# Performance work log

Measured on AMD Instinct MI355X. Metric: run time of the kernel, lower is better.

The kernel has to match this reference:

```python
import jax, jax.numpy as jnp
import numpy as np

B, T, C, H = 4, 2048, 768, 12
D = C // H  # head dim = 64

def setup_inputs() -> dict:
    key = jax.random.key(0)
    k1, k2, k3 = jax.random.split(key, 3)
    x = jax.random.normal(k1, (B, T, C), dtype=jnp.float32)
    W_attn = jax.random.normal(k2, (C, 3 * C), dtype=jnp.float32) * 0.02
    b_attn = jnp.zeros((3 * C,), dtype=jnp.float32)
    W_proj = jax.random.normal(k3, (C, C), dtype=jnp.float32) * 0.02
    b_proj = jnp.zeros((C,), dtype=jnp.float32)
    return {"x": x, "W_attn": W_attn, "b_attn": b_attn, "W_proj": W_proj, "b_proj": b_proj}

def reference(x, W_attn, b_attn, W_proj, b_proj):
    Bx, Tx, Cx = x.shape
    qkv = x @ W_attn + b_attn                      # [B,T,3C]
    q, k, v = jnp.split(qkv, 3, axis=2)
    q = q.reshape(Bx, Tx, H, D).swapaxes(1, 2)     # [B,H,T,D]
    k = k.reshape(Bx, Tx, H, D).swapaxes(1, 2)
    v = v.reshape(Bx, Tx, H, D).swapaxes(1, 2)
    att = jnp.einsum('bhqd,bhkd->bhqk', q, k) / jnp.sqrt(jnp.float32(D))
    mask = jnp.tril(jnp.ones((Tx, Tx), dtype=bool))
    att = jnp.where(mask, att, -jnp.inf)
    att = jax.nn.softmax(att, axis=-1)
    y = jnp.einsum('bhqk,bhkd->bhqd', att, v)      # [B,H,T,D]
    y = y.swapaxes(1, 2).reshape(Bx, Tx, Cx)
    return y @ W_proj + b_proj
```

## Files before the change

### kernel.cpp

```cpp
#include <hip/hip_runtime.h>
#include <hip/hip_bf16.h>

#define BATCH 4
#define TSEQ  2048
#define CDIM  768
#define HNUM  12
#define DHEAD 64
#define NQKV  (3*CDIM)
#define BTOT  (BATCH*TSEQ)
#define BH    (BATCH*HNUM)

typedef unsigned short u16;
typedef __attribute__((ext_vector_type(8))) __bf16 bf16x8;
typedef __attribute__((ext_vector_type(4))) float f32x4;

#define MFMA16(a,b,c) __builtin_amdgcn_mfma_f32_16x16x32_bf16((a),(b),(c),0,0,0)

__device__ __forceinline__ u16 f2b(float f) {
    union { float f; unsigned u; } v; v.f = f;
    unsigned u = v.u;
    unsigned r = (u + 0x7fffu + ((u >> 16) & 1u)) >> 16;
    return (u16)r;
}

__device__ __forceinline__ unsigned cvtpk(float lo, float hi) {
    unsigned r;
    asm("v_cvt_pk_bf16_f32 %0, %1, %2" : "=v"(r) : "v"(lo), "v"(hi));
    return r;
}

__device__ __forceinline__ float fexp2(float x) {
    float r;
    asm("v_exp_f32 %0, %1" : "=v"(r) : "v"(x));
    return r;
}

__device__ __forceinline__ void gload_lds(const void* g, void* l) {
    __builtin_amdgcn_global_load_lds(
        (const __attribute__((address_space(1))) void*)g,
        (__attribute__((address_space(3))) void*)l, 16, 0, 0);
}

__global__ __launch_bounds__(256) void cast_f32_bf16(
        const float* __restrict__ in, u16* __restrict__ out, int n4) {
    int i = blockIdx.x * blockDim.x + threadIdx.x;
    if (i >= n4) return;
    float4 a = reinterpret_cast<const float4*>(in)[i];
    ushort4 o;
    o.x = f2b(a.x); o.y = f2b(a.y); o.z = f2b(a.z); o.w = f2b(a.w);
    reinterpret_cast<ushort4*>(out)[i] = o;
}

__global__ __launch_bounds__(256) void tcast2(
        const float* __restrict__ Wa, const float* __restrict__ Wp,
        u16* __restrict__ WaT, u16* __restrict__ WpT) {
    __shared__ float tile[32][33];
    const float* in; u16* out; int Cc; int bx = blockIdx.x;
    if (bx < NQKV / 32) { in = Wa; out = WaT; Cc = NQKV; }
    else                { in = Wp; out = WpT; Cc = CDIM; bx -= NQKV / 32; }
    int c0 = bx * 32, r0 = blockIdx.y * 32;
    int tx = threadIdx.x, ty = threadIdx.y;
    #pragma unroll
    for (int i = 0; i < 32; i += 8)
        tile[ty + i][tx] = in[(size_t)(r0 + ty + i) * Cc + c0 + tx];
    __syncthreads();
    #pragma unroll
    for (int i = 0; i < 32; i += 8)
        out[(size_t)(c0 + ty + i) * CDIM + r0 + tx] = f2b(tile[tx][ty + i]);
}

template<int MODE, int NX>
__global__ __launch_bounds__(256) void gemm_bt(
        const u16* __restrict__ A, const u16* __restrict__ Bt,
        const float* __restrict__ bias,
        u16* __restrict__ qb, u16* __restrict__ kb, u16* __restrict__ vtb,
        float* __restrict__ outf, int K) {
    __shared__ u16 sA[2][128 * 32];
    __shared__ u16 sB[2][128 * 32];
    const int tid = threadIdx.x;
    const int lane = tid & 63;
    const int w = tid >> 6;
    const int wr = w >> 1, wc = w & 1;
    const int g = lane >> 4, lq = lane & 15;
    const int cpx = gridDim.x >> 3;
    const int wg = ((int)blockIdx.x & 7) * cpx + ((int)blockIdx.x >> 3);
    const int bx = wg % NX, by = wg / NX;
    const int m0 = by * 128, n0 = bx * 128;

    f32x4 acc[4][4] = {};

    auto stage = [&](int buf, int kt) {
        #pragma unroll
        for (int i = 0; i < 2; ++i) {
            int c = i * 256 + tid;
            int r = c >> 2, s = c & 3;
            int l = s ^ ((r >> 1) & 3);
            gload_lds(A  + (size_t)(m0 + r) * K + kt * 32 + l * 8, &sA[buf][c * 8]);
            gload_lds(Bt + (size_t)(n0 + r) * K + kt * 32 + l * 8, &sB[buf][c * 8]);
        }
    };

    const int KT = K / 32;
    stage(0, 0);
    __syncthreads();
    for (int kt = 0; kt < KT; ++kt) {
        if (kt + 1 < KT) stage((kt + 1) & 1, kt + 1);
        const u16* cA = sA[kt & 1];
        const u16* cB = sB[kt & 1];
        bf16x8 af[4], bfr[4];
        #pragma unroll
        for (int m = 0; m < 4; ++m) {
            int r = wr * 64 + m * 16 + lq;
            af[m] = *(const bf16x8*)&cA[r * 32 + ((g ^ ((r >> 1) & 3)) << 3)];
        }
        #pragma unroll
        for (int n = 0; n < 4; ++n) {
            int r = wc * 64 + n * 16 + lq;
            bfr[n] = *(const bf16x8*)&cB[r * 32 + ((g ^ ((r >> 1) & 3)) << 3)];
        }
        __builtin_amdgcn_s_setprio(1);
        #pragma unroll
        for (int m = 0; m < 4; ++m)
            #pragma unroll
            for (int n = 0; n < 4; ++n)
                acc[m][n] = MFMA16(bfr[n], af[m], acc[m][n]);
        __builtin_amdgcn_s_setprio(0);
        __syncthreads();
    }

    if (MODE == 0) {
        const int which = n0 / CDIM;
        #pragma unroll
        for (int m = 0; m < 4; ++m) {
            const int rg = m0 + wr * 64 + m * 16 + lq;
            const int b = rg >> 11, t = rg & (TSEQ - 1);
            #pragma unroll
            for (int n = 0; n < 4; ++n) {
                const int cg = n0 + wc * 64 + n * 16 + (g << 2);
                const int c  = cg - which * CDIM;
                const int h  = c >> 6, d = c & 63;
                const size_t bh = (size_t)(b * HNUM + h);
                const float4 bv = *(const float4*)&bias[cg];
                const float v0 = acc[m][n][0] + bv.x;
                const float v1 = acc[m][n][1] + bv.y;
                const float v2 = acc[m][n][2] + bv.z;
                const float v3 = acc[m][n][3] + bv.w;
                if (which == 0) {
                    const float s = 0.1803368801111243f;
                    ushort4 pv;
                    pv.x = f2b(v0 * s); pv.y = f2b(v1 * s);
                    pv.z = f2b(v2 * s); pv.w = f2b(v3 * s);
                    *(ushort4*)&qb[(bh * TSEQ + t) * DHEAD + d] = pv;
                } else if (which == 1) {
                    ushort4 pv;
                    pv.x = f2b(v0); pv.y = f2b(v1); pv.z = f2b(v2); pv.w = f2b(v3);
                    *(ushort4*)&kb[(bh * TSEQ + t) * DHEAD + d] = pv;
                } else {
                    vtb[(bh * DHEAD + d + 0) * TSEQ + t] = f2b(v0);
                    vtb[(bh * DHEAD + d + 1) * TSEQ + t] = f2b(v1);
                    vtb[(bh * DHEAD + d + 2) * TSEQ + t] = f2b(v2);
                    vtb[(bh * DHEAD + d + 3) * TSEQ + t] = f2b(v3);
                }
            }
        }
    } else {
        #pragma unroll
        for (int m = 0; m < 4; ++m) {
            const int rg = m0 + wr * 64 + m * 16 + lq;
            #pragma unroll
            for (int n = 0; n < 4; ++n) {
                const int cg = n0 + wc * 64 + n * 16 + (g << 2);
                const float4 bv = *(const float4*)&bias[cg];
                float4 ov;
                ov.x = acc[m][n][0] + bv.x;
                ov.y = acc[m][n][1] + bv.y;
                ov.z = acc[m][n][2] + bv.z;
                ov.w = acc[m][n][3] + bv.w;
                *(float4*)&outf[(size_t)rg * CDIM + cg] = ov;
            }
        }
    }
}

__global__ __launch_bounds__(256, 4) void attn_fwd(
        const u16* __restrict__ qb, const u16* __restrict__ kb,
        const u16* __restrict__ vtb, u16* __restrict__ yb) {
    __shared__ u16 sK[2][64 * 64];
    __shared__ u16 sVt[2][64 * 64];
    const int qt = 31 - (int)(blockIdx.x / BH);
    const int bh = blockIdx.x % BH;
    const int b = bh / HNUM, h = bh % HNUM;
    const int tid = threadIdx.x, lane = tid & 63, w = tid >> 6;
    const int g = lane >> 4, lq = lane & 15;
    const int qlo = qt * 64 + w * 16;
    const u16* qbase = qb  + (size_t)bh * TSEQ * DHEAD;
    const u16* kbase = kb  + (size_t)bh * TSEQ * DHEAD;
    const u16* vbase = vtb + (size_t)bh * DHEAD * TSEQ;

    bf16x8 qf[2];
    #pragma unroll
    for (int ks = 0; ks < 2; ++ks)
        qf[ks] = *(const bf16x8*)&qbase[(size_t)(qlo + lq) * DHEAD + ks * 32 + g * 8];

    union { unsigned u[4]; bf16x8 v; } ones;
    #pragma unroll
    for (int i = 0; i < 4; ++i) ones.u[i] = 0x3f803f80u;

    f32x4 o[4] = {};
    f32x4 ls = {};
    float mx = -__builtin_inff();

    auto STAGE = [&](int buf, int kt) {
        const int k0 = kt << 6;
        #pragma unroll
        for (int i = 0; i < 2; ++i) {
            int chunk = i * 256 + tid;
            int srow = chunk >> 3;
            int cb = ((chunk & 7) << 4) ^ ((srow & 7) << 4);
            gload_lds(kbase + (size_t)(k0 + srow) * DHEAD + (cb >> 1), &sK[buf][chunk * 8]);
            gload_lds(vbase + (size_t)srow * TSEQ + k0 + (cb >> 1),    &sVt[buf][chunk * 8]);
        }
    };

    const int nk = qt + 1;
    STAGE(0, 0);
    __syncthreads();
    for (int kt = 0; kt < nk; ++kt) {
        const int k0 = kt << 6;
        if (kt + 1 < nk) STAGE((kt + 1) & 1, kt + 1);
        const u16* cK = sK[kt & 1];
        const u16* cV = sVt[kt & 1];
        f32x4 s[4];
        #pragma unroll
        for (int n = 0; n < 4; ++n) s[n] = f32x4{0.f, 0.f, 0.f, 0.f};
        __builtin_amdgcn_s_setprio(1);
        #pragma unroll
        for (int n = 0; n < 4; ++n) {
            #pragma unroll
            for (int ks = 0; ks < 2; ++ks) {
                int r = n * 16 + lq;
                int lb = (r * 128 + (ks * 32 + g * 8) * 2) ^ ((r & 7) << 4);
                bf16x8 kf = *(const bf16x8*)((const char*)cK + lb);
                s[n] = MFMA16(kf, qf[ks], s[n]);
            }
        }
        __builtin_amdgcn_s_setprio(0);
        if (k0 + 63 > qlo) {
            const int qa = qlo + lq;
            #pragma unroll
            for (int n = 0; n < 4; ++n)
                #pragma unroll
                for (int j = 0; j < 4; ++j)
                    if (k0 + n * 16 + g * 4 + j > qa) s[n][j] = -__builtin_inff();
        }
        float t0 = fmaxf(fmaxf(s[0][0], s[0][1]), fmaxf(s[0][2], s[0][3]));
        float t1 = fmaxf(fmaxf(s[1][0], s[1][1]), fmaxf(s[1][2], s[1][3]));
        float t2 = fmaxf(fmaxf(s[2][0], s[2][1]), fmaxf(s[2][2], s[2][3]));
        float t3 = fmaxf(fmaxf(s[3][0], s[3][1]), fmaxf(s[3][2], s[3][3]));
        float tmax = fmaxf(fmaxf(t0, t1), fmaxf(t2, t3));
        tmax = fmaxf(tmax, __shfl_xor(tmax, 16));
        tmax = fmaxf(tmax, __shfl_xor(tmax, 32));
        if (__any(tmax > mx + 8.0f)) {
            float mnew = fmaxf(mx, tmax);
            float sc = fexp2(mx - mnew);
            mx = mnew;
            #pragma unroll
            for (int j = 0; j < 4; ++j) {
                float scj = __shfl(sc, (lane & 48) | ((g << 2) + j));
                ls[j] *= scj;
                #pragma unroll
                for (int n = 0; n < 4; ++n) o[n][j] *= scj;
            }
        }
        #pragma unroll
        for (int n = 0; n < 4; ++n)
            #pragma unroll
            for (int j = 0; j < 4; ++j)
                s[n][j] = fexp2(s[n][j] - mx);
        unsigned apk[4], bpk[4];
        #pragma unroll
        for (int n = 0; n < 4; ++n) {
            apk[n] = cvtpk(s[n][0], s[n][1]);
            bpk[n] = cvtpk(s[n][2], s[n][3]);
        }
        const int s0l = lq + ((lane & 16) << 1);
        const bool hi = (lane & 32) != 0;
        #pragma unroll
        for (int ks = 0; ks < 2; ++ks) {
            unsigned A0  = (unsigned)__shfl((int)apk[2 * ks],     s0l);
            unsigned B0  = (unsigned)__shfl((int)bpk[2 * ks],     s0l);
            unsigned A1  = (unsigned)__shfl((int)apk[2 * ks + 1], s0l);
            unsigned B1  = (unsigned)__shfl((int)bpk[2 * ks + 1], s0l);
            unsigned A0h = (unsigned)__shfl((int)apk[2 * ks],     s0l + 16);
            unsigned B0h = (unsigned)__shfl((int)bpk[2 * ks],     s0l + 16);
            unsigned A1h = (unsigned)__shfl((int)apk[2 * ks + 1], s0l + 16);
            unsigned B1h = (unsigned)__shfl((int)bpk[2 * ks + 1], s0l + 16);
            union { unsigned u[4]; bf16x8 v; } pa;
            pa.u[0] = hi ? A1  : A0;
            pa.u[1] = hi ? B1  : B0;
            pa.u[2] = hi ? A1h : A0h;
            pa.u[3] = hi ? B1h : B0h;
            __builtin_amdgcn_s_setprio(1);
            #pragma unroll
            for (int n = 0; n < 4; ++n) {
                int d = n * 16 + lq;
                int lb = (d * 128 + (ks * 32 + g * 8) * 2) ^ ((d & 7) << 4);
                bf16x8 vf = *(const bf16x8*)((const char*)cV + lb);
                o[n] = MFMA16(pa.v, vf, o[n]);
            }
            ls = MFMA16(pa.v, ones.v, ls);
            __builtin_amdgcn_s_setprio(0);
        }
        __syncthreads();
    }

    #pragma unroll
    for (int j = 0; j < 4; ++j) {
        float inv = 1.f / ls[j];
        const int t = qlo + g * 4 + j;
        #pragma unroll
        for (int n = 0; n < 4; ++n) {
            const int c = h * DHEAD + n * 16 + lq;
            yb[((size_t)b * TSEQ + t) * CDIM + c] = f2b(o[n][j] * inv);
        }
    }
}

extern "C" void kernel_launch(void* const* d_in, const int* in_sizes, int n_in,
                              void* d_out, int out_size, void* d_ws, size_t ws_size,
                              hipStream_t stream) {
    const float* x      = (const float*)d_in[0];
    const float* W_attn = (const float*)d_in[1];
    const float* b_attn = (const float*)d_in[2];
    const float* W_proj = (const float*)d_in[3];
    const float* b_proj = (const float*)d_in[4];
    float* out = (float*)d_out;

    u16* ws = (u16*)d_ws;
    u16* xb     = ws;
    u16* yb     = xb;
    u16* WattnT = xb     + (size_t)BTOT * CDIM;
    u16* WprojT = WattnT + (size_t)NQKV * CDIM;
    u16* qb     = WprojT + (size_t)CDIM * CDIM;
    u16* kb     = qb     + (size_t)BH * TSEQ * DHEAD;
    u16* vtb    = kb     + (size_t)BH * TSEQ * DHEAD;

    int n4 = BTOT * CDIM / 4;
    cast_f32_bf16<<<(n4 + 255) / 256, 256, 0, stream>>>(x, xb, n4);
    tcast2<<<dim3(NQKV / 32 + CDIM / 32, CDIM / 32), dim3(32, 8), 0, stream>>>(
        W_attn, W_proj, WattnT, WprojT);

    gemm_bt<0, NQKV / 128><<<dim3((NQKV / 128) * (BTOT / 128)), 256, 0, stream>>>(
        xb, WattnT, b_attn, qb, kb, vtb, nullptr, CDIM);

    attn_fwd<<<dim3((TSEQ / 64) * BH), 256, 0, stream>>>(qb, kb, vtb, yb);

    gemm_bt<1, CDIM / 128><<<dim3((CDIM / 128) * (BTOT / 128)), 256, 0, stream>>>(
        yb, WprojT, b_proj, nullptr, nullptr, nullptr, out, CDIM);
}
```

Before: 141.7 us.

## Double attention query tile per block and merge prep casts into one kernel

The attention kernel now gives each block 128 query rows instead of 64, and each wave handles two 16-row query subtiles. Every K/V tile staged in LDS is therefore reused for twice as many queries, halving K/V global traffic per query, and waves whose rows lie entirely before a key tile skip its compute. The x cast and the weight transpose-casts are merged into one launch to remove a kernel launch. In exchange the grid has half as many blocks, the causal work is less evenly balanced, and register pressure rises, which may reduce occupancy.

```diff
diff --git a/kernel.cpp b/kernel.cpp
--- a/kernel.cpp
+++ b/kernel.cpp
@@ -41,25 +41,31 @@
         (__attribute__((address_space(3))) void*)l, 16, 0, 0);
 }
 
-__global__ __launch_bounds__(256) void cast_f32_bf16(
-        const float* __restrict__ in, u16* __restrict__ out, int n4) {
-    int i = blockIdx.x * blockDim.x + threadIdx.x;
-    if (i >= n4) return;
-    float4 a = reinterpret_cast<const float4*>(in)[i];
-    ushort4 o;
-    o.x = f2b(a.x); o.y = f2b(a.y); o.z = f2b(a.z); o.w = f2b(a.w);
-    reinterpret_cast<ushort4*>(out)[i] = o;
-}
-
-__global__ __launch_bounds__(256) void tcast2(
+#define CAST_BLKS (BTOT * CDIM / 4 / 256)
+#define TA_BLKS   ((NQKV / 32) * (CDIM / 32))
+#define TP_BLKS   ((CDIM / 32) * (CDIM / 32))
+__global__ __launch_bounds__(256) void prep(
+        const float* __restrict__ x, u16* __restrict__ xb,
         const float* __restrict__ Wa, const float* __restrict__ Wp,
         u16* __restrict__ WaT, u16* __restrict__ WpT) {
     __shared__ float tile[32][33];
-    const float* in; u16* out; int Cc; int bx = blockIdx.x;
-    if (bx < NQKV / 32) { in = Wa; out = WaT; Cc = NQKV; }
-    else                { in = Wp; out = WpT; Cc = CDIM; bx -= NQKV / 32; }
-    int c0 = bx * 32, r0 = blockIdx.y * 32;
-    int tx = threadIdx.x, ty = threadIdx.y;
+    const int bx = blockIdx.x, tid = threadIdx.x;
+    if (bx < CAST_BLKS) {
+        int i = bx * 256 + tid;
+        float4 a = reinterpret_cast<const float4*>(x)[i];
+        ushort4 o;
+        o.x = f2b(a.x); o.y = f2b(a.y); o.z = f2b(a.z); o.w = f2b(a.w);
+        reinterpret_cast<ushort4*>(xb)[i] = o;
+        return;
+    }
+    int bz = bx - CAST_BLKS;
+    const float* in; u16* out; int Cc;
+    int nxa = NQKV / 32;
+    int cx, ry;
+    if (bz < TA_BLKS) { in = Wa; out = WaT; Cc = NQKV; cx = bz % nxa; ry = bz / nxa; }
+    else { bz -= TA_BLKS; in = Wp; out = WpT; Cc = CDIM; cx = bz % (CDIM/32); ry = bz / (CDIM/32); }
+    int c0 = cx * 32, r0 = ry * 32;
+    int tx = tid & 31, ty = tid >> 5;
     #pragma unroll
     for (int i = 0; i < 32; i += 8)
         tile[ty + i][tx] = in[(size_t)(r0 + ty + i) * Cc + c0 + tx];
@@ -187,28 +193,31 @@
         const u16* __restrict__ vtb, u16* __restrict__ yb) {
     __shared__ u16 sK[2][64 * 64];
     __shared__ u16 sVt[2][64 * 64];
-    const int qt = 31 - (int)(blockIdx.x / BH);
+    const int qt = 15 - (int)(blockIdx.x / BH);
     const int bh = blockIdx.x % BH;
     const int b = bh / HNUM, h = bh % HNUM;
     const int tid = threadIdx.x, lane = tid & 63, w = tid >> 6;
     const int g = lane >> 4, lq = lane & 15;
-    const int qlo = qt * 64 + w * 16;
+    const int qlo = qt * 128 + w * 32;
     const u16* qbase = qb  + (size_t)bh * TSEQ * DHEAD;
     const u16* kbase = kb  + (size_t)bh * TSEQ * DHEAD;
     const u16* vbase = vtb + (size_t)bh * DHEAD * TSEQ;
 
-    bf16x8 qf[2];
-    #pragma unroll
-    for (int ks = 0; ks < 2; ++ks)
-        qf[ks] = *(const bf16x8*)&qbase[(size_t)(qlo + lq) * DHEAD + ks * 32 + g * 8];
+    bf16x8 qf[2][2];
+    #pragma unroll
+    for (int m = 0; m < 2; ++m)
+        #pragma unroll
+        for (int ks = 0; ks < 2; ++ks)
+            qf[m][ks] = *(const bf16x8*)&qbase[(size_t)(qlo + m * 16 + lq) * DHEAD
+                                               + ks * 32 + g * 8];
 
     union { unsigned u[4]; bf16x8 v; } ones;
     #pragma unroll
     for (int i = 0; i < 4; ++i) ones.u[i] = 0x3f803f80u;
 
-    f32x4 o[4] = {};
-    f32x4 ls = {};
-    float mx = -__builtin_inff();
+    f32x4 o[2][4] = {};
+    f32x4 ls[2] = {};
+    float mx[2] = { -__builtin_inff(), -__builtin_inff() };
 
     auto STAGE = [&](int buf, int kt) {
         const int k0 = kt << 6;
@@ -222,108 +231,132 @@
         }
     };
 
-    const int nk = qt + 1;
+    const int nk = 2 * qt + 2;
     STAGE(0, 0);
     __syncthreads();
     for (int kt = 0; kt < nk; ++kt) {
         const int k0 = kt << 6;
         if (kt + 1 < nk) STAGE((kt + 1) & 1, kt + 1);
-        const u16* cK = sK[kt & 1];
-        const u16* cV = sVt[kt & 1];
-        f32x4 s[4];
-        #pragma unroll
-        for (int n = 0; n < 4; ++n) s[n] = f32x4{0.f, 0.f, 0.f, 0.f};
-        __builtin_amdgcn_s_setprio(1);
-        #pragma unroll
-        for (int n = 0; n < 4; ++n) {
+        if (k0 <= qlo + 31) {
+            const u16* cK = sK[kt & 1];
+            const u16* cV = sVt[kt & 1];
+            f32x4 s[2][4];
+            #pragma unroll
+            for (int m = 0; m < 2; ++m)
+                #pragma unroll
+                for (int n = 0; n < 4; ++n) s[m][n] = f32x4{0.f, 0.f, 0.f, 0.f};
+            __builtin_amdgcn_s_setprio(1);
+            #pragma unroll
+            for (int n = 0; n < 4; ++n) {
+                #pragma unroll
+                for (int ks = 0; ks < 2; ++ks) {
+                    int r = n * 16 + lq;
+                    int lb = (r * 128 + (ks * 32 + g * 8) * 2) ^ ((r & 7) << 4);
+                    bf16x8 kf = *(const bf16x8*)((const char*)cK + lb);
+                    s[0][n] = MFMA16(kf, qf[0][ks], s[0][n]);
+                    s[1][n] = MFMA16(kf, qf[1][ks], s[1][n]);
+                }
+            }
+            __builtin_amdgcn_s_setprio(0);
+            if (k0 + 63 > qlo) {
+                #pragma unroll
+                for (int m = 0; m < 2; ++m) {
+                    const int qa = qlo + m * 16 + lq;
+                    #pragma unroll
+                    for (int n = 0; n < 4; ++n)
+                        #pragma unroll
+                        for (int j = 0; j < 4; ++j)
+                            if (k0 + n * 16 + g * 4 + j > qa) s[m][n][j] = -__builtin_inff();
+                }
+            }
+            float tmax[2];
+            #pragma unroll
+            for (int m = 0; m < 2; ++m) {
+                float t0 = fmaxf(fmaxf(s[m][0][0], s[m][0][1]), fmaxf(s[m][0][2], s[m][0][3]));
+                float t1 = fmaxf(fmaxf(s[m][1][0], s[m][1][1]), fmaxf(s[m][1][2], s[m][1][3]));
+                float t2 = fmaxf(fmaxf(s[m][2][0], s[m][2][1]), fmaxf(s[m][2][2], s[m][2][3]));
+                float t3 = fmaxf(fmaxf(s[m][3][0], s[m][3][1]), fmaxf(s[m][3][2], s[m][3][3]));
+                float tm = fmaxf(fmaxf(t0, t1), fmaxf(t2, t3));
+                tm = fmaxf(tm, __shfl_xor(tm, 16));
+                tm = fmaxf(tm, __shfl_xor(tm, 32));
+                tmax[m] = tm;
+            }
+            if (__any(tmax[0] > mx[0] + 8.0f || tmax[1] > mx[1] + 8.0f)) {
+                #pragma unroll
+                for (int m = 0; m < 2; ++m) {
+                    float mnew = fmaxf(mx[m], tmax[m]);
+                    float sc = fexp2(mx[m] - mnew);
+                    mx[m] = mnew;
+                    #pragma unroll
+                    for (int j = 0; j < 4; ++j) {
+                        float scj = __shfl(sc, (lane & 48) | ((g << 2) + j));
+                        ls[m][j] *= scj;
+                        #pragma unroll
+                        for (int n = 0; n < 4; ++n) o[m][n][j] *= scj;
+                    }
+                }
+            }
+            unsigned apk[2][4], bpk[2][4];
+            #pragma unroll
+            for (int m = 0; m < 2; ++m)
+                #pragma unroll
+                for (int n = 0; n < 4; ++n) {
+                    float p0 = fexp2(s[m][n][0] - mx[m]);
+                    float p1 = fexp2(s[m][n][1] - mx[m]);
+                    float p2 = fexp2(s[m][n][2] - mx[m]);
+                    float p3 = fexp2(s[m][n][3] - mx[m]);
+                    apk[m][n] = cvtpk(p0, p1);
+                    bpk[m][n] = cvtpk(p2, p3);
+                }
+            const int s0l = lq + ((lane & 16) << 1);
+            const bool hi = (lane & 32) != 0;
             #pragma unroll
             for (int ks = 0; ks < 2; ++ks) {
-                int r = n * 16 + lq;
-                int lb = (r * 128 + (ks * 32 + g * 8) * 2) ^ ((r & 7) << 4);
-                bf16x8 kf = *(const bf16x8*)((const char*)cK + lb);
-                s[n] = MFMA16(kf, qf[ks], s[n]);
-            }
-        }
-        __builtin_amdgcn_s_setprio(0);
-        if (k0 + 63 > qlo) {
-            const int qa = qlo + lq;
-            #pragma unroll
-            for (int n = 0; n < 4; ++n)
-                #pragma unroll
-                for (int j = 0; j < 4; ++j)
-                    if (k0 + n * 16 + g * 4 + j > qa) s[n][j] = -__builtin_inff();
-        }
-        float t0 = fmaxf(fmaxf(s[0][0], s[0][1]), fmaxf(s[0][2], s[0][3]));
-        float t1 = fmaxf(fmaxf(s[1][0], s[1][1]), fmaxf(s[1][2], s[1][3]));
-        float t2 = fmaxf(fmaxf(s[2][0], s[2][1]), fmaxf(s[2][2], s[2][3]));
-        float t3 = fmaxf(fmaxf(s[3][0], s[3][1]), fmaxf(s[3][2], s[3][3]));
-        float tmax = fmaxf(fmaxf(t0, t1), fmaxf(t2, t3));
-        tmax = fmaxf(tmax, __shfl_xor(tmax, 16));
-        tmax = fmaxf(tmax, __shfl_xor(tmax, 32));
-        if (__any(tmax > mx + 8.0f)) {
-            float mnew = fmaxf(mx, tmax);
-            float sc = fexp2(mx - mnew);
-            mx = mnew;
-            #pragma unroll
-            for (int j = 0; j < 4; ++j) {
-                float scj = __shfl(sc, (lane & 48) | ((g << 2) + j));
-                ls[j] *= scj;
-                #pragma unroll
-                for (int n = 0; n < 4; ++n) o[n][j] *= scj;
-            }
-        }
-        #pragma unroll
-        for (int n = 0; n < 4; ++n)
-            #pragma unroll
-            for (int j = 0; j < 4; ++j)
-                s[n][j] = fexp2(s[n][j] - mx);
-        unsigned apk[4], bpk[4];
-        #pragma unroll
-        for (int n = 0; n < 4; ++n) {
-            apk[n] = cvtpk(s[n][0], s[n][1]);
-            bpk[n] = cvtpk(s[n][2], s[n][3]);
-        }
-        const int s0l = lq + ((lane & 16) << 1);
-        const bool hi = (lane & 32) != 0;
-        #pragma unroll
-        for (int ks = 0; ks < 2; ++ks) {
-            unsigned A0  = (unsigned)__shfl((int)apk[2 * ks],     s0l);
-            unsigned B0  = (unsigned)__shfl((int)bpk[2 * ks],     s0l);
-            unsigned A1  = (unsigned)__shfl((int)apk[2 * ks + 1], s0l);
-            unsigned B1  = (unsigned)__shfl((int)bpk[2 * ks + 1], s0l);
-            unsigned A0h = (unsigned)__shfl((int)apk[2 * ks],     s0l + 16);
-            unsigned B0h = (unsigned)__shfl((int)bpk[2 * ks],     s0l + 16);
-            unsigned A1h = (unsigned)__shfl((int)apk[2 * ks + 1], s0l + 16);
-            unsigned B1h = (unsigned)__shfl((int)bpk[2 * ks + 1], s0l + 16);
-            union { unsigned u[4]; bf16x8 v; } pa;
-            pa.u[0] = hi ? A1  : A0;
-            pa.u[1] = hi ? B1  : B0;
-            pa.u[2] = hi ? A1h : A0h;
-            pa.u[3] = hi ? B1h : B0h;
-            __builtin_amdgcn_s_setprio(1);
-            #pragma unroll
-            for (int n = 0; n < 4; ++n) {
-                int d = n * 16 + lq;
-                int lb = (d * 128 + (ks * 32 + g * 8) * 2) ^ ((d & 7) << 4);
-                bf16x8 vf = *(const bf16x8*)((const char*)cV + lb);
-                o[n] = MFMA16(pa.v, vf, o[n]);
-            }
-            ls = MFMA16(pa.v, ones.v, ls);
-            __builtin_amdgcn_s_setprio(0);
+                union { unsigned u[4]; bf16x8 v; } pa[2];
+                #pragma unroll
+                for (int m = 0; m < 2; ++m) {
+                    unsigned A0  = (unsigned)__shfl((int)apk[m][2 * ks],     s0l);
+                    unsigned B0  = (unsigned)__shfl((int)bpk[m][2 * ks],     s0l);
+                    unsigned A1  = (unsigned)__shfl((int)apk[m][2 * ks + 1], s0l);
+                    unsigned B1  = (unsigned)__shfl((int)bpk[m][2 * ks + 1], s0l);
+                    unsigned A0h = (unsigned)__shfl((int)apk[m][2 * ks],     s0l + 16);
+                    unsigned B0h = (unsigned)__shfl((int)bpk[m][2 * ks],     s0l + 16);
+                    unsigned A1h = (unsigned)__shfl((int)apk[m][2 * ks + 1], s0l + 16);
+                    unsigned B1h = (unsigned)__shfl((int)bpk[m][2 * ks + 1], s0l + 16);
+                    pa[m].u[0] = hi ? A1  : A0;
+                    pa[m].u[1] = hi ? B1  : B0;
+                    pa[m].u[2] = hi ? A1h : A0h;
+                    pa[m].u[3] = hi ? B1h : B0h;
+                }
+                __builtin_amdgcn_s_setprio(1);
+                #pragma unroll
+                for (int n = 0; n < 4; ++n) {
+                    int d = n * 16 + lq;
+                    int lb = (d * 128 + (ks * 32 + g * 8) * 2) ^ ((d & 7) << 4);
+                    bf16x8 vf = *(const bf16x8*)((const char*)cV + lb);
+                    o[0][n] = MFMA16(pa[0].v, vf, o[0][n]);
+                    o[1][n] = MFMA16(pa[1].v, vf, o[1][n]);
+                }
+                ls[0] = MFMA16(pa[0].v, ones.v, ls[0]);
+                ls[1] = MFMA16(pa[1].v, ones.v, ls[1]);
+                __builtin_amdgcn_s_setprio(0);
+            }
         }
         __syncthreads();
     }
 
     #pragma unroll
-    for (int j = 0; j < 4; ++j) {
-        float inv = 1.f / ls[j];
-        const int t = qlo + g * 4 + j;
-        #pragma unroll
-        for (int n = 0; n < 4; ++n) {
-            const int c = h * DHEAD + n * 16 + lq;
-            yb[((size_t)b * TSEQ + t) * CDIM + c] = f2b(o[n][j] * inv);
-        }
-    }
+    for (int m = 0; m < 2; ++m)
+        #pragma unroll
+        for (int j = 0; j < 4; ++j) {
+            float inv = 1.f / ls[m][j];
+            const int t = qlo + m * 16 + g * 4 + j;
+            #pragma unroll
+            for (int n = 0; n < 4; ++n) {
+                const int c = h * DHEAD + n * 16 + lq;
+                yb[((size_t)b * TSEQ + t) * CDIM + c] = f2b(o[m][n][j] * inv);
+            }
+        }
 }
 
 extern "C" void kernel_launch(void* const* d_in, const int* in_sizes, int n_in,
@@ -345,15 +378,13 @@
     u16* kb     = qb     + (size_t)BH * TSEQ * DHEAD;
     u16* vtb    = kb     + (size_t)BH * TSEQ * DHEAD;
 
-    int n4 = BTOT * CDIM / 4;
-    cast_f32_bf16<<<(n4 + 255) / 256, 256, 0, stream>>>(x, xb, n4);
-    tcast2<<<dim3(NQKV / 32 + CDIM / 32, CDIM / 32), dim3(32, 8), 0, stream>>>(
-        W_attn, W_proj, WattnT, WprojT);
+    prep<<<dim3(CAST_BLKS + TA_BLKS + TP_BLKS), 256, 0, stream>>>(
+        x, xb, W_attn, W_proj, WattnT, WprojT);
 
     gemm_bt<0, NQKV / 128><<<dim3((NQKV / 128) * (BTOT / 128)), 256, 0, stream>>>(
         xb, WattnT, b_attn, qb, kb, vtb, nullptr, CDIM);
 
-    attn_fwd<<<dim3((TSEQ / 64) * BH), 256, 0, stream>>>(qb, kb, vtb, yb);
+    attn_fwd<<<dim3((TSEQ / 128) * BH), 256, 0, stream>>>(qb, kb, vtb, yb);
 
     gemm_bt<1, CDIM / 128><<<dim3((CDIM / 128) * (BTOT / 128)), 256, 0, stream>>>(
         yb, WprojT, b_proj, nullptr, nullptr, nullptr, out, CDIM);
```

Result: slower. 165.7 us (+17.0%).
